# Performance work log

Measured on AMD Instinct MI355X. Metric: run time of the kernel, lower is better.

Reference implementation:

```python
import jax, jax.numpy as jnp
import numpy as np

EPS = 1e-6
R = 2          # filter half-width (length=2 -> 5x5 directional filters)
TAU = 0.1
PI = float(np.pi)

# ---- kernels (all single-channel, OIHW) ----
_SOBEL_X = jnp.array([[-1., 0., 1.], [-2., 0., 2.], [-1., 0., 1.]], dtype=jnp.float32)[None, None] / 8.0  # kornia normalized sobel
_SOBEL_Y = jnp.transpose(_SOBEL_X, (0, 1, 3, 2))

def _gauss_kernel5():
    x = jnp.arange(5, dtype=jnp.float32) - 2.0
    g = jnp.exp(-(x * x) / (2.0 * 4.0))  # sigma = 2
    g = g / g.sum()
    return (g[:, None] * g[None, :])[None, None]  # (1,1,5,5)

def _dir_filters():
    k = 2 * R + 1
    horiz = np.zeros((k, k), np.float32); horiz[R, :] = 1.0
    vert = np.zeros((k, k), np.float32); vert[:, R] = 1.0
    cnt_diag = np.eye(k, dtype=np.float32)
    lead_diag = np.fliplr(np.eye(k)).astype(np.float32)
    return [jnp.asarray(f)[None, None] for f in (horiz, vert, lead_diag, cnt_diag)]

def _conv(x, k, padding):
    # cross-correlation, NCHW / OIHW (matches F.conv2d)
    return jax.lax.conv_general_dilated(x, k, (1, 1), padding,
                                        dimension_numbers=('NCHW', 'OIHW', 'NCHW'))

def _conv_padded(x, k, pad, mode):
    x = jnp.pad(x, ((0, 0), (0, 0), (pad, pad), (pad, pad)), mode=mode)
    return _conv(x, k, 'VALID')

def _normal_angles(img):
    # img: (B,1,H,W). kornia gaussian_blur2d: reflect pad; spatial_gradient: replicate pad.
    blur = _conv_padded(img, _gauss_kernel5(), 2, 'reflect')
    gx = _conv_padded(blur, _SOBEL_X, 1, 'edge')
    gy = _conv_padded(blur, _SOBEL_Y, 1, 'edge')
    grad_xx = _conv_padded(gx, _SOBEL_X, 1, 'edge')
    grad_xy = _conv_padded(gy, _SOBEL_X, 1, 'edge')
    grad_yy = _conv_padded(gy, _SOBEL_Y, 1, 'edge')
    angle = jnp.arctan(grad_yy * jnp.sign(-(grad_xy + EPS)) / (grad_xx + EPS))
    return angle[:, 0]  # (B,H,W)

def _section_masks(a):
    horiz = ((a >= -PI / 8) & (a < PI / 8)).astype(jnp.float32)
    vert = (((a >= 3 * PI / 8) & (a < PI / 2)) | ((a >= -PI / 2) & (a < -3 * PI / 8))).astype(jnp.float32)
    lead = ((a >= PI / 8) & (a < 3 * PI / 8)).astype(jnp.float32)
    cnt = ((a >= -3 * PI / 8) & (a < -PI / 8)).astype(jnp.float32)
    return [horiz, vert, lead, cnt]

def setup_inputs() -> dict:
    key = jax.random.key(0)
    k1, k2 = jax.random.split(key)
    predictions = jax.random.uniform(k1, (1, 1, 2048, 2048), dtype=jnp.float32)
    labels = jax.random.uniform(k2, (1, 2048, 2048), dtype=jnp.float32)
    return {"predictions": predictions, "labels": labels}

def reference(predictions, labels):
    true_angles = _normal_angles(labels[:, None])           # (B,H,W)
    # NOTE: original also computes pred_angles = get_normal_anlges(predictions),
    # but it is dead code (never used), so it is omitted.
    exp_preds = jnp.exp(predictions / TAU)                   # (B,1,H,W)
    masks = _section_masks(true_angles)
    pad = [(R, R), (R, R)]
    loss = jnp.zeros_like(exp_preds)
    for filt, mask in zip(_dir_filters(), masks):
        resp = _conv(exp_preds, filt, pad)                   # zero-padded directional sum
        norm = exp_preds / (resp + EPS)
        loss = loss + jnp.log(norm) * mask                   # mask (B,H,W) broadcasts over channel
    return -jnp.mean(loss)
```

## Files before the change

### kernel.cpp

```cpp
#include <hip/hip_runtime.h>
#include <math.h>

#define HH 2048
#define WW 2048
#define T 8

#define GW0 0.15246914402033867f
#define GW1 0.22184129554377693f
#define GW2 0.25137912086578894f

typedef float f4 __attribute__((ext_vector_type(4)));

struct R8 { float v[8]; };
struct R6 { float v[6]; };

__device__ __forceinline__ R8 hrow(const float* __restrict__ lab, int vr, int xb,
                                   bool edgew, bool le, bool re) {
    int r = vr < 0 ? -vr : (vr >= HH ? 2 * HH - 2 - vr : vr);
    const float* row = lab + (size_t)r * WW;
    f4 A = *(const f4*)(row + max(xb - 4, 0));
    f4 B = *(const f4*)(row + xb);
    f4 C = *(const f4*)(row + min(xb + 4, WW - 4));
    float w[12] = {A.x, A.y, A.z, A.w, B.x, B.y, B.z, B.w, C.x, C.y, C.z, C.w};
    if (edgew) {
        if (le) { w[0] = C.x; w[1] = B.w; w[2] = B.z; w[3] = B.y; }
        if (re) { w[8] = B.z; w[9] = B.y; w[10] = B.x; w[11] = A.w; }
    }
    R8 h;
    #pragma unroll
    for (int j = 0; j < 8; ++j)
        h.v[j] = GW0 * (w[j] + w[j + 4]) + GW1 * (w[j + 1] + w[j + 3]) + GW2 * w[j + 2];
    return h;
}

__device__ __forceinline__ R8 vg(const R8& a, const R8& b, const R8& c, const R8& d, const R8& e_,
                                 bool edgew, bool le, bool re) {
    R8 o;
    #pragma unroll
    for (int j = 0; j < 8; ++j)
        o.v[j] = GW0 * (a.v[j] + e_.v[j]) + GW1 * (b.v[j] + d.v[j]) + GW2 * c.v[j];
    if (edgew) {
        if (le) { o.v[0] = o.v[2]; o.v[1] = o.v[2]; }
        if (re) { o.v[6] = o.v[5]; o.v[7] = o.v[5]; }
    }
    return o;
}

__device__ __forceinline__ void sobel(const R8& u, const R8& m, const R8& d, R6& ox, R6& oy,
                                      bool edgew, bool le, bool re) {
    #pragma unroll
    for (int j = 0; j < 6; ++j) {
        ox.v[j] = ((u.v[j+2] - u.v[j]) + 2.f*(m.v[j+2] - m.v[j]) + (d.v[j+2] - d.v[j])) * 0.125f;
        oy.v[j] = ((d.v[j] - u.v[j]) + 2.f*(d.v[j+1] - u.v[j+1]) + (d.v[j+2] - u.v[j+2])) * 0.125f;
    }
    if (edgew) {
        if (le) { ox.v[0] = ox.v[1]; oy.v[0] = oy.v[1]; }
        if (re) { ox.v[5] = ox.v[4]; oy.v[5] = oy.v[4]; }
    }
}

__device__ __forceinline__ R8 erow(const float* __restrict__ pred, int ry, int xb,
                                   bool edgew, bool le, bool re) {
    R8 o;
    if (ry < 0 || ry >= HH) {
        #pragma unroll
        for (int j = 0; j < 8; ++j) o.v[j] = 0.f;
        return o;
    }
    const float* row = pred + (size_t)ry * WW;
    f4 A = *(const f4*)(row + max(xb - 4, 0));
    f4 B = *(const f4*)(row + xb);
    f4 C = *(const f4*)(row + min(xb + 4, WW - 4));
    float w[8] = {A.z, A.w, B.x, B.y, B.z, B.w, C.x, C.y};
    #pragma unroll
    for (int j = 0; j < 8; ++j) o.v[j] = __expf(w[j] * 10.f);
    if (edgew) {
        if (le) { o.v[0] = 0.f; o.v[1] = 0.f; }
        if (re) { o.v[6] = 0.f; o.v[7] = 0.f; }
    }
    return o;
}

__global__ __launch_bounds__(256, 2) void steal_main(const float* __restrict__ pred,
                                                     const float* __restrict__ lab,
                                                     float* __restrict__ acc) {
    const int lane = threadIdx.x & 63;
    const int wid  = (blockIdx.x << 2) + (threadIdx.x >> 6);
    const int sx = wid & 7;
    const int y0 = (wid >> 3) * T;
    const int xb = sx * 256 + lane * 4;
    const bool edgew = (sx == 0) || (sx == 7);
    const bool le = (sx == 0) && (lane == 0);
    const bool re = (sx == 7) && (lane == 63);

    const float T1f = 0.41421356237309503f;
    const float T3f = 2.41421356237309510f;

    R8 A0 = hrow(lab, y0-4, xb, edgew, le, re);
    R8 A1 = hrow(lab, y0-3, xb, edgew, le, re);
    R8 A2 = hrow(lab, y0-2, xb, edgew, le, re);
    R8 A3 = hrow(lab, y0-1, xb, edgew, le, re);
    R8 H0 = hrow(lab, y0+0, xb, edgew, le, re);
    R8 H1 = hrow(lab, y0+1, xb, edgew, le, re);
    R8 H2 = hrow(lab, y0+2, xb, edgew, le, re);
    R8 H3 = hrow(lab, y0+3, xb, edgew, le, re);
    R8 bm2 = vg(A0, A1, A2, A3, H0, edgew, le, re);
    R8 bm1 = vg(A1, A2, A3, H0, H1, edgew, le, re);
    R8 b0  = vg(A2, A3, H0, H1, H2, edgew, le, re);
    R8 b1  = vg(A3, H0, H1, H2, H3, edgew, le, re);
    R6 gx0, gy0, gx1, gy1;
    if (y0 > 0) {
        sobel(bm2, bm1, b0, gx0, gy0, edgew, le, re);
        sobel(bm1, b0,  b1, gx1, gy1, edgew, le, re);
    } else {
        sobel(b0, b0, b1, gx1, gy1, edgew, le, re);
        gx0 = gx1; gy0 = gy1;
    }
    R8 e0 = erow(pred, y0-2, xb, edgew, le, re);
    R8 e1 = erow(pred, y0-1, xb, edgew, le, re);
    R8 e2 = erow(pred, y0+0, xb, edgew, le, re);
    R8 e3 = erow(pred, y0+1, xb, edgew, le, re);

    float lsum = 0.f;

    for (int i = 0; i < T; ++i) {
        const int y = y0 + i;

        R8 bn;
        if (y + 2 < HH) {
            R8 hn = hrow(lab, y + 4, xb, edgew, le, re);
            bn = vg(H0, H1, H2, H3, hn, edgew, le, re);
            H0 = H1; H1 = H2; H2 = H3; H3 = hn;
        } else bn = b1;

        R6 gxn, gyn;
        if (y + 1 < HH) sobel(b0, b1, bn, gxn, gyn, edgew, le, re);
        else { gxn = gx1; gyn = gy1; }

        R8 en = erow(pred, y + 2, xb, edgew, le, re);

        f4 pc4 = *(const f4*)(pred + (size_t)y * WW + xb);
        float pcv[4] = {pc4.x, pc4.y, pc4.z, pc4.w};

        #pragma unroll
        for (int k = 0; k < 4; ++k) {
            float gxx = ((gx0.v[k+2]-gx0.v[k]) + 2.f*(gx1.v[k+2]-gx1.v[k]) +
                         (gxn.v[k+2]-gxn.v[k])) * 0.125f;
            float gxy = ((gy0.v[k+2]-gy0.v[k]) + 2.f*(gy1.v[k+2]-gy1.v[k]) +
                         (gyn.v[k+2]-gyn.v[k])) * 0.125f;
            float gyy = ((gyn.v[k]-gy0.v[k]) + 2.f*(gyn.v[k+1]-gy0.v[k+1]) +
                         (gyn.v[k+2]-gy0.v[k+2])) * 0.125f;
            float sg = -(gxy + 1e-6f);
            float sgn = (sg > 0.f) ? 1.f : ((sg < 0.f) ? -1.f : 0.f);
            float rt = gyy * sgn * __builtin_amdgcn_rcpf(gxx + 1e-6f);

            float hs  = e2.v[k] + e2.v[k+1] + e2.v[k+2] + e2.v[k+3] + e2.v[k+4];
            float vs  = e0.v[k+2] + e1.v[k+2] + e2.v[k+2] + e3.v[k+2] + en.v[k+2];
            float dls = e0.v[k]   + e1.v[k+1] + e2.v[k+2] + e3.v[k+3] + en.v[k+4];
            float dcs = e0.v[k+4] + e1.v[k+3] + e2.v[k+2] + e3.v[k+1] + en.v[k];

            bool isH = (rt >= -T1f) && (rt < T1f);
            bool isL = (rt >=  T1f) && (rt < T3f);
            bool isC = (rt >= -T3f) && (rt < -T1f);
            bool has = isH || isL || isC || (rt >= T3f) || (rt < -T3f);
            float resp = isH ? hs : (isL ? dls : (isC ? dcs : vs));
            float lv = pcv[k] * 10.f - __logf(resp + 1e-6f);
            lsum += has ? lv : 0.f;
        }

        b0 = b1; b1 = bn;
        gx0 = gx1; gx1 = gxn; gy0 = gy1; gy1 = gyn;
        e0 = e1; e1 = e2; e2 = e3; e3 = en;
    }

    #pragma unroll
    for (int off = 32; off; off >>= 1) lsum += __shfl_down(lsum, off, 64);
    if (lane == 0) acc[wid] = lsum;
}

__global__ __launch_bounds__(256) void steal_finalize(const float* __restrict__ acc,
                                                      float* __restrict__ out, int n) {
    __shared__ double sd[256];
    double a = 0.0;
    int n4 = n >> 2;
    for (int i = threadIdx.x; i < n4; i += 256) {
        f4 v = *(const f4*)(acc + i * 4);
        a += (double)v.x + (double)v.y + (double)v.z + (double)v.w;
    }
    for (int i = (n4 << 2) + threadIdx.x; i < n; i += 256) a += (double)acc[i];
    sd[threadIdx.x] = a;
    __syncthreads();
    for (int s = 128; s > 0; s >>= 1) {
        if (threadIdx.x < s) sd[threadIdx.x] += sd[threadIdx.x + s];
        __syncthreads();
    }
    if (threadIdx.x == 0) out[0] = (float)(-sd[0] / 4194304.0);
}

extern "C" void kernel_launch(void* const* d_in, const int* in_sizes, int n_in,
                              void* d_out, int out_size, void* d_ws, size_t ws_size,
                              hipStream_t stream) {
    const float* pred = (const float*)d_in[0];
    const float* lab  = (const float*)d_in[1];
    float* out = (float*)d_out;
    float* ws  = (float*)d_ws;

    const int nwaves = 8 * (HH / T);
    const int nblocks = nwaves / 4;

    steal_main<<<nblocks, 256, 0, stream>>>(pred, lab, ws);
    steal_finalize<<<1, 256, 0, stream>>>(ws, out, nwaves);
}
```

Before: 36.29 us.

## Stage exp(pred) rows in a per-wave LDS ring buffer and prefetch next rows

Each exp(pred/tau) value is now computed once per row and stored in a per-wave shared-memory ring of 8 rows, with halo entries written by the edge lanes. Previously each lane computed 8 exponentials per row for 4 output pixels. Loads of the next label and prediction rows are issued one iteration ahead, and the loop is fully unrolled. Rows per wave drop from 8 to 4 and the occupancy hint rises to 4 blocks, which roughly doubles the per-wave recomputation of the label blur halo. The centre term now comes from a log of the stored exponential instead of the raw prediction, which adds one log per pixel.

```diff
diff --git a/kernel.cpp b/kernel.cpp
--- a/kernel.cpp
+++ b/kernel.cpp
@@ -3,28 +3,40 @@
 
 #define HH 2048
 #define WW 2048
-#define T 8
+#define T 4
+#define RING_STRIDE 264
+#define RING_F (8 * RING_STRIDE)
 
 #define GW0 0.15246914402033867f
 #define GW1 0.22184129554377693f
 #define GW2 0.25137912086578894f
 
-typedef float f4 __attribute__((ext_vector_type(4)));
+typedef float f2v __attribute__((ext_vector_type(2)));
+typedef float f4  __attribute__((ext_vector_type(4)));
 
 struct R8 { float v[8]; };
 struct R6 { float v[6]; };
-
-__device__ __forceinline__ R8 hrow(const float* __restrict__ lab, int vr, int xb,
-                                   bool edgew, bool le, bool re) {
-    int r = vr < 0 ? -vr : (vr >= HH ? 2 * HH - 2 - vr : vr);
-    const float* row = lab + (size_t)r * WW;
-    f4 A = *(const f4*)(row + max(xb - 4, 0));
-    f4 B = *(const f4*)(row + xb);
-    f4 C = *(const f4*)(row + min(xb + 4, WW - 4));
-    float w[12] = {A.x, A.y, A.z, A.w, B.x, B.y, B.z, B.w, C.x, C.y, C.z, C.w};
+struct Raw { f4 a, b, c; };
+
+__device__ __forceinline__ int reflect_row(int vr) {
+    return vr < 0 ? -vr : (vr >= HH ? 2 * HH - 2 - vr : vr);
+}
+
+__device__ __forceinline__ Raw load_row3(const float* __restrict__ p, int r, int xb) {
+    const float* row = p + (size_t)r * WW;
+    Raw o;
+    o.a = *(const f4*)(row + max(xb - 4, 0));
+    o.b = *(const f4*)(row + xb);
+    o.c = *(const f4*)(row + min(xb + 4, WW - 4));
+    return o;
+}
+
+__device__ __forceinline__ R8 make_h(const Raw& R, bool edgew, bool le, bool re) {
+    float w[12] = {R.a.x, R.a.y, R.a.z, R.a.w, R.b.x, R.b.y, R.b.z, R.b.w,
+                   R.c.x, R.c.y, R.c.z, R.c.w};
     if (edgew) {
-        if (le) { w[0] = C.x; w[1] = B.w; w[2] = B.z; w[3] = B.y; }
-        if (re) { w[8] = B.z; w[9] = B.y; w[10] = B.x; w[11] = A.w; }
+        if (le) { w[0] = R.c.x; w[1] = R.b.w; w[2] = R.b.z; w[3] = R.b.y; }
+        if (re) { w[8] = R.b.z; w[9] = R.b.y; w[10] = R.b.x; w[11] = R.a.w; }
     }
     R8 h;
     #pragma unroll
@@ -59,88 +71,149 @@
     }
 }
 
-__device__ __forceinline__ R8 erow(const float* __restrict__ pred, int ry, int xb,
-                                   bool edgew, bool le, bool re) {
+__device__ __forceinline__ void ewrite(float* __restrict__ ring, int slot, int lane,
+                                       const f4& pv, const f2v& pl, const f2v& pr,
+                                       bool zrow, bool lzero, bool rzero) {
+    float* rp = ring + slot * RING_STRIDE;
+    if (!zrow) {
+        f4 ev;
+        ev.x = __expf(pv.x * 10.f); ev.y = __expf(pv.y * 10.f);
+        ev.z = __expf(pv.z * 10.f); ev.w = __expf(pv.w * 10.f);
+        *(f4*)(rp + 4 + 4 * lane) = ev;
+        if (lane == 0) {
+            f2v h2; h2.x = lzero ? 0.f : __expf(pl.x * 10.f);
+                    h2.y = lzero ? 0.f : __expf(pl.y * 10.f);
+            *(f2v*)(rp + 2) = h2;
+        }
+        if (lane == 63) {
+            f2v h2; h2.x = rzero ? 0.f : __expf(pr.x * 10.f);
+                    h2.y = rzero ? 0.f : __expf(pr.y * 10.f);
+            *(f2v*)(rp + 260) = h2;
+        }
+    } else {
+        f4 z = {0.f, 0.f, 0.f, 0.f};
+        *(f4*)(rp + 4 + 4 * lane) = z;
+        if (lane == 0)  { f2v z2 = {0.f, 0.f}; *(f2v*)(rp + 2) = z2; }
+        if (lane == 63) { f2v z2 = {0.f, 0.f}; *(f2v*)(rp + 260) = z2; }
+    }
+}
+
+__device__ __forceinline__ R8 eread(const float* __restrict__ ring, int slot, int lane) {
+    const float* rp = ring + slot * RING_STRIDE + 4 * lane;
+    f2v w01 = *(const f2v*)(rp + 2);
+    f4  w25 = *(const f4*)(rp + 4);
+    f2v w67 = *(const f2v*)(rp + 8);
     R8 o;
-    if (ry < 0 || ry >= HH) {
-        #pragma unroll
-        for (int j = 0; j < 8; ++j) o.v[j] = 0.f;
-        return o;
-    }
-    const float* row = pred + (size_t)ry * WW;
-    f4 A = *(const f4*)(row + max(xb - 4, 0));
-    f4 B = *(const f4*)(row + xb);
-    f4 C = *(const f4*)(row + min(xb + 4, WW - 4));
-    float w[8] = {A.z, A.w, B.x, B.y, B.z, B.w, C.x, C.y};
-    #pragma unroll
-    for (int j = 0; j < 8; ++j) o.v[j] = __expf(w[j] * 10.f);
-    if (edgew) {
-        if (le) { o.v[0] = 0.f; o.v[1] = 0.f; }
-        if (re) { o.v[6] = 0.f; o.v[7] = 0.f; }
-    }
+    o.v[0] = w01.x; o.v[1] = w01.y; o.v[2] = w25.x; o.v[3] = w25.y;
+    o.v[4] = w25.z; o.v[5] = w25.w; o.v[6] = w67.x; o.v[7] = w67.y;
     return o;
 }
 
-__global__ __launch_bounds__(256, 2) void steal_main(const float* __restrict__ pred,
+__global__ __launch_bounds__(256, 4) void steal_main(const float* __restrict__ pred,
                                                      const float* __restrict__ lab,
                                                      float* __restrict__ acc) {
+    __shared__ float ring_s[4 * RING_F];
     const int lane = threadIdx.x & 63;
-    const int wid  = (blockIdx.x << 2) + (threadIdx.x >> 6);
+    const int warp = threadIdx.x >> 6;
+    const int wid  = (blockIdx.x << 2) + warp;
     const int sx = wid & 7;
     const int y0 = (wid >> 3) * T;
     const int xb = sx * 256 + lane * 4;
     const bool edgew = (sx == 0) || (sx == 7);
     const bool le = (sx == 0) && (lane == 0);
     const bool re = (sx == 7) && (lane == 63);
+    const bool lzero = (sx == 0), rzero = (sx == 7);
+    float* ring = ring_s + warp * RING_F;
 
     const float T1f = 0.41421356237309503f;
     const float T3f = 2.41421356237309510f;
 
-    R8 A0 = hrow(lab, y0-4, xb, edgew, le, re);
-    R8 A1 = hrow(lab, y0-3, xb, edgew, le, re);
-    R8 A2 = hrow(lab, y0-2, xb, edgew, le, re);
-    R8 A3 = hrow(lab, y0-1, xb, edgew, le, re);
-    R8 H0 = hrow(lab, y0+0, xb, edgew, le, re);
-    R8 H1 = hrow(lab, y0+1, xb, edgew, le, re);
-    R8 H2 = hrow(lab, y0+2, xb, edgew, le, re);
-    R8 H3 = hrow(lab, y0+3, xb, edgew, le, re);
-    R8 bm2 = vg(A0, A1, A2, A3, H0, edgew, le, re);
-    R8 bm1 = vg(A1, A2, A3, H0, H1, edgew, le, re);
-    R8 b0  = vg(A2, A3, H0, H1, H2, edgew, le, re);
-    R8 b1  = vg(A3, H0, H1, H2, H3, edgew, le, re);
+    R8 H0, H1, H2, H3, b0, b1;
     R6 gx0, gy0, gx1, gy1;
-    if (y0 > 0) {
-        sobel(bm2, bm1, b0, gx0, gy0, edgew, le, re);
-        sobel(bm1, b0,  b1, gx1, gy1, edgew, le, re);
-    } else {
-        sobel(b0, b0, b1, gx1, gy1, edgew, le, re);
-        gx0 = gx1; gy0 = gy1;
-    }
-    R8 e0 = erow(pred, y0-2, xb, edgew, le, re);
-    R8 e1 = erow(pred, y0-1, xb, edgew, le, re);
-    R8 e2 = erow(pred, y0+0, xb, edgew, le, re);
-    R8 e3 = erow(pred, y0+1, xb, edgew, le, re);
+    {
+        Raw r0 = load_row3(lab, reflect_row(y0 - 4), xb);
+        Raw r1 = load_row3(lab, reflect_row(y0 - 3), xb);
+        Raw r2 = load_row3(lab, reflect_row(y0 - 2), xb);
+        Raw r3 = load_row3(lab, reflect_row(y0 - 1), xb);
+        R8 A0 = make_h(r0, edgew, le, re);
+        R8 A1 = make_h(r1, edgew, le, re);
+        R8 A2 = make_h(r2, edgew, le, re);
+        R8 A3 = make_h(r3, edgew, le, re);
+        Raw r4 = load_row3(lab, y0 + 0, xb);
+        Raw r5 = load_row3(lab, y0 + 1, xb);
+        Raw r6 = load_row3(lab, y0 + 2, xb);
+        Raw r7 = load_row3(lab, y0 + 3, xb);
+        H0 = make_h(r4, edgew, le, re);
+        H1 = make_h(r5, edgew, le, re);
+        H2 = make_h(r6, edgew, le, re);
+        H3 = make_h(r7, edgew, le, re);
+        R8 bm2 = vg(A0, A1, A2, A3, H0, edgew, le, re);
+        R8 bm1 = vg(A1, A2, A3, H0, H1, edgew, le, re);
+        b0 = vg(A2, A3, H0, H1, H2, edgew, le, re);
+        b1 = vg(A3, H0, H1, H2, H3, edgew, le, re);
+        if (y0 > 0) {
+            sobel(bm2, bm1, b0, gx0, gy0, edgew, le, re);
+            sobel(bm1, b0,  b1, gx1, gy1, edgew, le, re);
+        } else {
+            sobel(b0, b0, b1, gx1, gy1, edgew, le, re);
+            gx0 = gx1; gy0 = gy1;
+        }
+    }
+
+    #pragma unroll
+    for (int j = 0; j < 4; ++j) {
+        int ry = y0 - 2 + j;
+        bool zrow = (ry < 0);
+        const float* prow = pred + (size_t)max(ry, 0) * WW;
+        f4 pv = *(const f4*)(prow + xb);
+        f2v pl = {0.f, 0.f}, pr = {0.f, 0.f};
+        if (lane == 0)  pl = *(const f2v*)(prow + max(xb - 2, 0));
+        if (lane == 63) pr = *(const f2v*)(prow + min(xb + 4, WW - 2));
+        ewrite(ring, (ry + 4) & 7, lane, pv, pl, pr, zrow, lzero, rzero);
+    }
+
+    Raw nlab = load_row3(lab, reflect_row(y0 + 4), xb);
+    f4 npred; f2v npl = {0.f, 0.f}, npr = {0.f, 0.f};
+    {
+        const float* prow = pred + (size_t)min(y0 + 2, HH - 1) * WW;
+        npred = *(const f4*)(prow + xb);
+        if (lane == 0)  npl = *(const f2v*)(prow + max(xb - 2, 0));
+        if (lane == 63) npr = *(const f2v*)(prow + min(xb + 4, WW - 2));
+    }
 
     float lsum = 0.f;
 
+    #pragma unroll
     for (int i = 0; i < T; ++i) {
         const int y = y0 + i;
 
         R8 bn;
         if (y + 2 < HH) {
-            R8 hn = hrow(lab, y + 4, xb, edgew, le, re);
+            R8 hn = make_h(nlab, edgew, le, re);
             bn = vg(H0, H1, H2, H3, hn, edgew, le, re);
             H0 = H1; H1 = H2; H2 = H3; H3 = hn;
         } else bn = b1;
 
+        ewrite(ring, (y + 6) & 7, lane, npred, npl, npr, (y + 2 >= HH), lzero, rzero);
+
+        if (i < T - 1) {
+            nlab = load_row3(lab, reflect_row(y + 5), xb);
+            const float* prow = pred + (size_t)min(y + 3, HH - 1) * WW;
+            npred = *(const f4*)(prow + xb);
+            npl.x = 0.f; npl.y = 0.f; npr.x = 0.f; npr.y = 0.f;
+            if (lane == 0)  npl = *(const f2v*)(prow + max(xb - 2, 0));
+            if (lane == 63) npr = *(const f2v*)(prow + min(xb + 4, WW - 2));
+        }
+
         R6 gxn, gyn;
         if (y + 1 < HH) sobel(b0, b1, bn, gxn, gyn, edgew, le, re);
         else { gxn = gx1; gyn = gy1; }
 
-        R8 en = erow(pred, y + 2, xb, edgew, le, re);
-
-        f4 pc4 = *(const f4*)(pred + (size_t)y * WW + xb);
-        float pcv[4] = {pc4.x, pc4.y, pc4.z, pc4.w};
+        R8 wA = eread(ring, (y + 2) & 7, lane);
+        R8 wB = eread(ring, (y + 3) & 7, lane);
+        R8 wC = eread(ring, (y + 4) & 7, lane);
+        R8 wD = eread(ring, (y + 5) & 7, lane);
+        R8 wE = eread(ring, (y + 6) & 7, lane);
 
         #pragma unroll
         for (int k = 0; k < 4; ++k) {
@@ -154,23 +227,23 @@
             float sgn = (sg > 0.f) ? 1.f : ((sg < 0.f) ? -1.f : 0.f);
             float rt = gyy * sgn * __builtin_amdgcn_rcpf(gxx + 1e-6f);
 
-            float hs  = e2.v[k] + e2.v[k+1] + e2.v[k+2] + e2.v[k+3] + e2.v[k+4];
-            float vs  = e0.v[k+2] + e1.v[k+2] + e2.v[k+2] + e3.v[k+2] + en.v[k+2];
-            float dls = e0.v[k]   + e1.v[k+1] + e2.v[k+2] + e3.v[k+3] + en.v[k+4];
-            float dcs = e0.v[k+4] + e1.v[k+3] + e2.v[k+2] + e3.v[k+1] + en.v[k];
+            float hs  = wC.v[k] + wC.v[k+1] + wC.v[k+2] + wC.v[k+3] + wC.v[k+4];
+            float vs  = wA.v[k+2] + wB.v[k+2] + wC.v[k+2] + wD.v[k+2] + wE.v[k+2];
+            float dls = wA.v[k]   + wB.v[k+1] + wC.v[k+2] + wD.v[k+3] + wE.v[k+4];
+            float dcs = wA.v[k+4] + wB.v[k+3] + wC.v[k+2] + wD.v[k+1] + wE.v[k];
 
             bool isH = (rt >= -T1f) && (rt < T1f);
             bool isL = (rt >=  T1f) && (rt < T3f);
             bool isC = (rt >= -T3f) && (rt < -T1f);
             bool has = isH || isL || isC || (rt >= T3f) || (rt < -T3f);
             float resp = isH ? hs : (isL ? dls : (isC ? dcs : vs));
-            float lv = pcv[k] * 10.f - __logf(resp + 1e-6f);
+            float lc = __logf(wC.v[k+2]);
+            float lv = lc - __logf(resp + 1e-6f);
             lsum += has ? lv : 0.f;
         }
 
         b0 = b1; b1 = bn;
         gx0 = gx1; gx1 = gxn; gy0 = gy1; gy1 = gyn;
-        e0 = e1; e1 = e2; e2 = e3; e3 = en;
     }
 
     #pragma unroll
```

Measured after the change: 133.5 us. +268.0%, slower.

## Split fused kernel into section-code pass and loss pass with smaller row tiles

Applied to the files above, without the earlier changes.

Breaks the single fused kernel into two. The first computes the blur, Hessian and angle section per pixel and writes a byte code to workspace. The second reads those codes together with the predictions to compute the directional sums and the log loss. The row tile also drops from 8 to 4, which doubles the number of waves and the halo recomputation. The intent is lower register pressure and more parallelism per kernel, at the cost of an extra 4 MB write and read of the codes and one more kernel launch.

```diff
diff --git a/kernel.cpp b/kernel.cpp
--- a/kernel.cpp
+++ b/kernel.cpp
@@ -1,30 +1,41 @@
 #include <hip/hip_runtime.h>
 #include <math.h>
+#include <stdint.h>
 
 #define HH 2048
 #define WW 2048
-#define T 8
+#define T 4
 
 #define GW0 0.15246914402033867f
 #define GW1 0.22184129554377693f
 #define GW2 0.25137912086578894f
 
-typedef float f4 __attribute__((ext_vector_type(4)));
+typedef float f2v __attribute__((ext_vector_type(2)));
+typedef float f4  __attribute__((ext_vector_type(4)));
 
 struct R8 { float v[8]; };
 struct R6 { float v[6]; };
-
-__device__ __forceinline__ R8 hrow(const float* __restrict__ lab, int vr, int xb,
-                                   bool edgew, bool le, bool re) {
-    int r = vr < 0 ? -vr : (vr >= HH ? 2 * HH - 2 - vr : vr);
-    const float* row = lab + (size_t)r * WW;
-    f4 A = *(const f4*)(row + max(xb - 4, 0));
-    f4 B = *(const f4*)(row + xb);
-    f4 C = *(const f4*)(row + min(xb + 4, WW - 4));
-    float w[12] = {A.x, A.y, A.z, A.w, B.x, B.y, B.z, B.w, C.x, C.y, C.z, C.w};
-    if (edgew) {
-        if (le) { w[0] = C.x; w[1] = B.w; w[2] = B.z; w[3] = B.y; }
-        if (re) { w[8] = B.z; w[9] = B.y; w[10] = B.x; w[11] = A.w; }
+struct Raw { f4 a, b, c; };
+
+__device__ __forceinline__ int reflect_row(int vr) {
+    return vr < 0 ? -vr : (vr >= HH ? 2 * HH - 2 - vr : vr);
+}
+
+__device__ __forceinline__ Raw load_row3(const float* __restrict__ p, int r, int xb) {
+    const float* row = p + (size_t)r * WW;
+    Raw o;
+    o.a = *(const f4*)(row + max(xb - 4, 0));
+    o.b = *(const f4*)(row + xb);
+    o.c = *(const f4*)(row + min(xb + 4, WW - 4));
+    return o;
+}
+
+__device__ __forceinline__ R8 make_h(const Raw& R, bool edgew, bool le, bool re) {
+    float w[12] = {R.a.x, R.a.y, R.a.z, R.a.w, R.b.x, R.b.y, R.b.z, R.b.w,
+                   R.c.x, R.c.y, R.c.z, R.c.w};
+    if (edgew) {
+        if (le) { w[0] = R.c.x; w[1] = R.b.w; w[2] = R.b.z; w[3] = R.b.y; }
+        if (re) { w[8] = R.b.z; w[9] = R.b.y; w[10] = R.b.x; w[11] = R.a.w; }
     }
     R8 h;
     #pragma unroll
@@ -81,9 +92,8 @@
     return o;
 }
 
-__global__ __launch_bounds__(256, 2) void steal_main(const float* __restrict__ pred,
-                                                     const float* __restrict__ lab,
-                                                     float* __restrict__ acc) {
+__global__ __launch_bounds__(256) void steal_sections(const float* __restrict__ lab,
+                                                      uint32_t* __restrict__ codes) {
     const int lane = threadIdx.x & 63;
     const int wid  = (blockIdx.x << 2) + (threadIdx.x >> 6);
     const int sx = wid & 7;
@@ -96,39 +106,45 @@
     const float T1f = 0.41421356237309503f;
     const float T3f = 2.41421356237309510f;
 
-    R8 A0 = hrow(lab, y0-4, xb, edgew, le, re);
-    R8 A1 = hrow(lab, y0-3, xb, edgew, le, re);
-    R8 A2 = hrow(lab, y0-2, xb, edgew, le, re);
-    R8 A3 = hrow(lab, y0-1, xb, edgew, le, re);
-    R8 H0 = hrow(lab, y0+0, xb, edgew, le, re);
-    R8 H1 = hrow(lab, y0+1, xb, edgew, le, re);
-    R8 H2 = hrow(lab, y0+2, xb, edgew, le, re);
-    R8 H3 = hrow(lab, y0+3, xb, edgew, le, re);
-    R8 bm2 = vg(A0, A1, A2, A3, H0, edgew, le, re);
-    R8 bm1 = vg(A1, A2, A3, H0, H1, edgew, le, re);
-    R8 b0  = vg(A2, A3, H0, H1, H2, edgew, le, re);
-    R8 b1  = vg(A3, H0, H1, H2, H3, edgew, le, re);
+    R8 H0, H1, H2, H3, b0, b1;
     R6 gx0, gy0, gx1, gy1;
-    if (y0 > 0) {
-        sobel(bm2, bm1, b0, gx0, gy0, edgew, le, re);
-        sobel(bm1, b0,  b1, gx1, gy1, edgew, le, re);
-    } else {
-        sobel(b0, b0, b1, gx1, gy1, edgew, le, re);
-        gx0 = gx1; gy0 = gy1;
-    }
-    R8 e0 = erow(pred, y0-2, xb, edgew, le, re);
-    R8 e1 = erow(pred, y0-1, xb, edgew, le, re);
-    R8 e2 = erow(pred, y0+0, xb, edgew, le, re);
-    R8 e3 = erow(pred, y0+1, xb, edgew, le, re);
-
-    float lsum = 0.f;
-
+    {
+        Raw r0 = load_row3(lab, reflect_row(y0 - 4), xb);
+        Raw r1 = load_row3(lab, reflect_row(y0 - 3), xb);
+        Raw r2 = load_row3(lab, reflect_row(y0 - 2), xb);
+        Raw r3 = load_row3(lab, reflect_row(y0 - 1), xb);
+        R8 A0 = make_h(r0, edgew, le, re);
+        R8 A1 = make_h(r1, edgew, le, re);
+        R8 A2 = make_h(r2, edgew, le, re);
+        R8 A3 = make_h(r3, edgew, le, re);
+        Raw r4 = load_row3(lab, y0 + 0, xb);
+        Raw r5 = load_row3(lab, y0 + 1, xb);
+        Raw r6 = load_row3(lab, y0 + 2, xb);
+        Raw r7 = load_row3(lab, y0 + 3, xb);
+        H0 = make_h(r4, edgew, le, re);
+        H1 = make_h(r5, edgew, le, re);
+        H2 = make_h(r6, edgew, le, re);
+        H3 = make_h(r7, edgew, le, re);
+        R8 bm2 = vg(A0, A1, A2, A3, H0, edgew, le, re);
+        R8 bm1 = vg(A1, A2, A3, H0, H1, edgew, le, re);
+        b0 = vg(A2, A3, H0, H1, H2, edgew, le, re);
+        b1 = vg(A3, H0, H1, H2, H3, edgew, le, re);
+        if (y0 > 0) {
+            sobel(bm2, bm1, b0, gx0, gy0, edgew, le, re);
+            sobel(bm1, b0,  b1, gx1, gy1, edgew, le, re);
+        } else {
+            sobel(b0, b0, b1, gx1, gy1, edgew, le, re);
+            gx0 = gx1; gy0 = gy1;
+        }
+    }
+
+    #pragma unroll
     for (int i = 0; i < T; ++i) {
         const int y = y0 + i;
 
         R8 bn;
         if (y + 2 < HH) {
-            R8 hn = hrow(lab, y + 4, xb, edgew, le, re);
+            R8 hn = make_h(load_row3(lab, reflect_row(y + 4), xb), edgew, le, re);
             bn = vg(H0, H1, H2, H3, hn, edgew, le, re);
             H0 = H1; H1 = H2; H2 = H3; H3 = hn;
         } else bn = b1;
@@ -137,11 +153,7 @@
         if (y + 1 < HH) sobel(b0, b1, bn, gxn, gyn, edgew, le, re);
         else { gxn = gx1; gyn = gy1; }
 
-        R8 en = erow(pred, y + 2, xb, edgew, le, re);
-
-        f4 pc4 = *(const f4*)(pred + (size_t)y * WW + xb);
-        float pcv[4] = {pc4.x, pc4.y, pc4.z, pc4.w};
-
+        uint32_t cw = 0;
         #pragma unroll
         for (int k = 0; k < 4; ++k) {
             float gxx = ((gx0.v[k+2]-gx0.v[k]) + 2.f*(gx1.v[k+2]-gx1.v[k]) +
@@ -154,22 +166,61 @@
             float sgn = (sg > 0.f) ? 1.f : ((sg < 0.f) ? -1.f : 0.f);
             float rt = gyy * sgn * __builtin_amdgcn_rcpf(gxx + 1e-6f);
 
+            bool isH = (rt >= -T1f) && (rt < T1f);
+            bool isL = (rt >=  T1f) && (rt < T3f);
+            bool isC = (rt >= -T3f) && (rt < -T1f);
+            bool isV = (rt >= T3f) || (rt < -T3f);
+            uint32_t c = isH ? 0u : (isL ? 1u : (isC ? 2u : (isV ? 3u : 4u)));
+            cw |= c << (8 * k);
+        }
+        codes[((size_t)y * WW + xb) >> 2] = cw;
+
+        b0 = b1; b1 = bn;
+        gx0 = gx1; gx1 = gxn; gy0 = gy1; gy1 = gyn;
+    }
+}
+
+__global__ __launch_bounds__(256) void steal_loss(const float* __restrict__ pred,
+                                                  const uint32_t* __restrict__ codes,
+                                                  float* __restrict__ acc) {
+    const int lane = threadIdx.x & 63;
+    const int wid  = (blockIdx.x << 2) + (threadIdx.x >> 6);
+    const int sx = wid & 7;
+    const int y0 = (wid >> 3) * T;
+    const int xb = sx * 256 + lane * 4;
+    const bool edgew = (sx == 0) || (sx == 7);
+    const bool le = (sx == 0) && (lane == 0);
+    const bool re = (sx == 7) && (lane == 63);
+
+    R8 e0 = erow(pred, y0 - 2, xb, edgew, le, re);
+    R8 e1 = erow(pred, y0 - 1, xb, edgew, le, re);
+    R8 e2 = erow(pred, y0 + 0, xb, edgew, le, re);
+    R8 e3 = erow(pred, y0 + 1, xb, edgew, le, re);
+
+    float lsum = 0.f;
+
+    #pragma unroll
+    for (int i = 0; i < T; ++i) {
+        const int y = y0 + i;
+        R8 en = erow(pred, y + 2, xb, edgew, le, re);
+
+        f4 pc4 = *(const f4*)(pred + (size_t)y * WW + xb);
+        float pcv[4] = {pc4.x, pc4.y, pc4.z, pc4.w};
+        uint32_t cw = codes[((size_t)y * WW + xb) >> 2];
+
+        #pragma unroll
+        for (int k = 0; k < 4; ++k) {
             float hs  = e2.v[k] + e2.v[k+1] + e2.v[k+2] + e2.v[k+3] + e2.v[k+4];
             float vs  = e0.v[k+2] + e1.v[k+2] + e2.v[k+2] + e3.v[k+2] + en.v[k+2];
             float dls = e0.v[k]   + e1.v[k+1] + e2.v[k+2] + e3.v[k+3] + en.v[k+4];
             float dcs = e0.v[k+4] + e1.v[k+3] + e2.v[k+2] + e3.v[k+1] + en.v[k];
 
-            bool isH = (rt >= -T1f) && (rt < T1f);
-            bool isL = (rt >=  T1f) && (rt < T3f);
-            bool isC = (rt >= -T3f) && (rt < -T1f);
-            bool has = isH || isL || isC || (rt >= T3f) || (rt < -T3f);
-            float resp = isH ? hs : (isL ? dls : (isC ? dcs : vs));
+            uint32_t c = (cw >> (8 * k)) & 0xffu;
+            float resp = (c == 0u) ? hs : ((c == 1u) ? dls : ((c == 2u) ? dcs : vs));
             float lv = pcv[k] * 10.f - __logf(resp + 1e-6f);
-            lsum += has ? lv : 0.f;
+            lsum += (c < 4u) ? lv : 0.f;
         }
 
-        b0 = b1; b1 = bn;
-        gx0 = gx1; gx1 = gxn; gy0 = gy1; gy1 = gyn;
         e0 = e1; e1 = e2; e2 = e3; e3 = en;
     }
 
@@ -203,11 +254,14 @@
     const float* pred = (const float*)d_in[0];
     const float* lab  = (const float*)d_in[1];
     float* out = (float*)d_out;
-    float* ws  = (float*)d_ws;
+
+    uint32_t* codes = (uint32_t*)d_ws;
+    float* accb = (float*)((uint8_t*)d_ws + (size_t)HH * WW);
 
     const int nwaves = 8 * (HH / T);
     const int nblocks = nwaves / 4;
 
-    steal_main<<<nblocks, 256, 0, stream>>>(pred, lab, ws);
-    steal_finalize<<<1, 256, 0, stream>>>(ws, out, nwaves);
-}
+    steal_sections<<<nblocks, 256, 0, stream>>>(lab, codes);
+    steal_loss<<<nblocks, 256, 0, stream>>>(pred, codes, accb);
+    steal_finalize<<<1, 256, 0, stream>>>(accb, out, nwaves);
+}
```

New measurement: 41.33 us. +13.9%, slower.

## Split into interior kernel without boundary checks and separate border kernel

Applied to the files above, without the earlier changes.

Moves the 4 top and 4 bottom rows into a small border kernel, so the interior kernel runs a fully unrolled 16-step software pipeline with no reflect or bounds branches and rotating register buffers. Sobel and the 3x3 second derivatives are factored into separable partial sums, and the horizontal 5-tap sum uses prefix sums to cut adds. This adds a third kernel launch and may raise register pressure because the launch_bounds occupancy hint was dropped.

```diff
diff --git a/kernel.cpp b/kernel.cpp
--- a/kernel.cpp
+++ b/kernel.cpp
@@ -3,7 +3,6 @@
 
 #define HH 2048
 #define WW 2048
-#define T 8
 
 #define GW0 0.15246914402033867f
 #define GW1 0.22184129554377693f
@@ -11,20 +10,20 @@
 
 typedef float f4 __attribute__((ext_vector_type(4)));
 
+#define NWI 2040
+#define NWB 16
+#define NACC (NWI + NWB)
+
 struct R8 { float v[8]; };
 struct R6 { float v[6]; };
-
-__device__ __forceinline__ R8 hrow(const float* __restrict__ lab, int vr, int xb,
-                                   bool edgew, bool le, bool re) {
-    int r = vr < 0 ? -vr : (vr >= HH ? 2 * HH - 2 - vr : vr);
-    const float* row = lab + (size_t)r * WW;
-    f4 A = *(const f4*)(row + max(xb - 4, 0));
-    f4 B = *(const f4*)(row + xb);
-    f4 C = *(const f4*)(row + min(xb + 4, WW - 4));
-    float w[12] = {A.x, A.y, A.z, A.w, B.x, B.y, B.z, B.w, C.x, C.y, C.z, C.w};
-    if (edgew) {
-        if (le) { w[0] = C.x; w[1] = B.w; w[2] = B.z; w[3] = B.y; }
-        if (re) { w[8] = B.z; w[9] = B.y; w[10] = B.x; w[11] = A.w; }
+struct Raw { f4 a, b, c; };
+
+__device__ __forceinline__ R8 make_h(const Raw& R, bool edgew, bool le, bool re) {
+    float w[12] = {R.a.x, R.a.y, R.a.z, R.a.w, R.b.x, R.b.y, R.b.z, R.b.w,
+                   R.c.x, R.c.y, R.c.z, R.c.w};
+    if (edgew) {
+        if (le) { w[0] = R.c.x; w[1] = R.b.w; w[2] = R.b.z; w[3] = R.b.y; }
+        if (re) { w[8] = R.b.z; w[9] = R.b.y; w[10] = R.b.x; w[11] = R.a.w; }
     }
     R8 h;
     #pragma unroll
@@ -33,8 +32,8 @@
     return h;
 }
 
-__device__ __forceinline__ R8 vg(const R8& a, const R8& b, const R8& c, const R8& d, const R8& e_,
-                                 bool edgew, bool le, bool re) {
+__device__ __forceinline__ R8 vg5(const R8& a, const R8& b, const R8& c, const R8& d, const R8& e_,
+                                  bool edgew, bool le, bool re) {
     R8 o;
     #pragma unroll
     for (int j = 0; j < 8; ++j)
@@ -46,8 +45,157 @@
     return o;
 }
 
-__device__ __forceinline__ void sobel(const R8& u, const R8& m, const R8& d, R6& ox, R6& oy,
-                                      bool edgew, bool le, bool re) {
+__device__ __forceinline__ void sobel1(const R8& u, const R8& m, const R8& d, R6& ox, R6& oy,
+                                       bool edgew, bool le, bool re) {
+    float E[8], F[8];
+    #pragma unroll
+    for (int j = 0; j < 8; ++j) {
+        E[j] = u.v[j] + 2.f * m.v[j] + d.v[j];
+        F[j] = d.v[j] - u.v[j];
+    }
+    #pragma unroll
+    for (int j = 0; j < 6; ++j) {
+        ox.v[j] = (E[j + 2] - E[j]) * 0.125f;
+        oy.v[j] = (F[j] + 2.f * F[j + 1] + F[j + 2]) * 0.125f;
+    }
+    if (edgew) {
+        if (le) { ox.v[0] = ox.v[1]; oy.v[0] = oy.v[1]; }
+        if (re) { ox.v[5] = ox.v[4]; oy.v[5] = oy.v[4]; }
+    }
+}
+
+__global__ __launch_bounds__(256) void steal_interior(const float* __restrict__ pred,
+                                                      const float* __restrict__ lab,
+                                                      float* __restrict__ acc) {
+    const int lane = threadIdx.x & 63;
+    const int wid  = (blockIdx.x << 2) + (threadIdx.x >> 6);
+    const int w  = wid & 7;
+    const int rg = wid >> 3;
+    const int y0 = 4 + rg * 8;
+    const int xb = w * 256 + lane * 4;
+    const int xl = max(xb - 4, 0);
+    const int xr = min(xb + 4, WW - 4);
+    const bool edgew = (w == 0) || (w == 7);
+    const bool le = (w == 0) && (lane == 0);
+    const bool re = (w == 7) && (lane == 63);
+
+    const float T1f = 0.41421356237309503f;
+    const float T3f = 2.41421356237309510f;
+
+    R8 h[5], bl[3], er[5];
+    R6 gzx[3], gzy[3];
+    float lsum = 0.f;
+
+    #pragma unroll
+    for (int s = 0; s < 16; ++s) {
+        {
+            const float* row = lab + (size_t)(y0 - 4 + s) * WW;
+            Raw rw;
+            rw.a = *(const f4*)(row + xl);
+            rw.b = *(const f4*)(row + xb);
+            rw.c = *(const f4*)(row + xr);
+            h[s % 5] = make_h(rw, edgew, le, re);
+        }
+
+        if (s >= 4) {
+            const int j = s - 4;
+            bl[j % 3] = vg5(h[j % 5], h[(j + 1) % 5], h[(j + 2) % 5],
+                            h[(j + 3) % 5], h[(j + 4) % 5], edgew, le, re);
+            const float* row = pred + (size_t)(y0 - 2 + j) * WW;
+            f4 A = *(const f4*)(row + xl);
+            f4 B = *(const f4*)(row + xb);
+            f4 C = *(const f4*)(row + xr);
+            float ww[8] = {A.z, A.w, B.x, B.y, B.z, B.w, C.x, C.y};
+            R8 e_;
+            #pragma unroll
+            for (int q = 0; q < 8; ++q) e_.v[q] = __expf(ww[q] * 10.f);
+            if (edgew) {
+                if (le) { e_.v[0] = 0.f; e_.v[1] = 0.f; }
+                if (re) { e_.v[6] = 0.f; e_.v[7] = 0.f; }
+            }
+            er[j % 5] = e_;
+        }
+
+        if (s >= 6) {
+            const int g = s - 6;
+            sobel1(bl[g % 3], bl[(g + 1) % 3], bl[(g + 2) % 3],
+                   gzx[g % 3], gzy[g % 3], edgew, le, re);
+        }
+
+        if (s >= 8) {
+            const int i = s - 8;
+            const R6& X0 = gzx[i % 3];
+            const R6& X1 = gzx[(i + 1) % 3];
+            const R6& X2 = gzx[(i + 2) % 3];
+            const R6& Y0 = gzy[i % 3];
+            const R6& Y1 = gzy[(i + 1) % 3];
+            const R6& Y2 = gzy[(i + 2) % 3];
+            float Cx[6], Cy[6], Dy[6];
+            #pragma unroll
+            for (int j = 0; j < 6; ++j) {
+                Cx[j] = X0.v[j] + 2.f * X1.v[j] + X2.v[j];
+                Cy[j] = Y0.v[j] + 2.f * Y1.v[j] + Y2.v[j];
+                Dy[j] = Y2.v[j] - Y0.v[j];
+            }
+            const R8& eA = er[i % 5];
+            const R8& eB = er[(i + 1) % 5];
+            const R8& eC = er[(i + 2) % 5];
+            const R8& eD = er[(i + 3) % 5];
+            const R8& eE = er[(i + 4) % 5];
+            float P[8];
+            P[0] = eC.v[0];
+            #pragma unroll
+            for (int j = 1; j < 8; ++j) P[j] = P[j - 1] + eC.v[j];
+
+            f4 pc4 = *(const f4*)(pred + (size_t)(y0 + i) * WW + xb);
+            float pcv[4] = {pc4.x, pc4.y, pc4.z, pc4.w};
+
+            #pragma unroll
+            for (int k = 0; k < 4; ++k) {
+                float gxx = (Cx[k + 2] - Cx[k]) * 0.125f;
+                float gxy = (Cy[k + 2] - Cy[k]) * 0.125f;
+                float gyy = (Dy[k] + 2.f * Dy[k + 1] + Dy[k + 2]) * 0.125f;
+
+                float sg = -(gxy + 1e-6f);
+                float sgn = (sg > 0.f) ? 1.f : ((sg < 0.f) ? -1.f : 0.f);
+                float rt = gyy * sgn * __builtin_amdgcn_rcpf(gxx + 1e-6f);
+
+                float hs  = (k == 0) ? P[4] : (P[k + 4] - P[k - 1]);
+                float vs  = eA.v[k+2] + eB.v[k+2] + eC.v[k+2] + eD.v[k+2] + eE.v[k+2];
+                float dls = eA.v[k]   + eB.v[k+1] + eC.v[k+2] + eD.v[k+3] + eE.v[k+4];
+                float dcs = eA.v[k+4] + eB.v[k+3] + eC.v[k+2] + eD.v[k+1] + eE.v[k];
+
+                bool isH = (rt >= -T1f) && (rt < T1f);
+                bool isL = (rt >=  T1f) && (rt < T3f);
+                bool isC = (rt >= -T3f) && (rt < -T1f);
+                bool has = isH || isL || isC || (rt >= T3f) || (rt < -T3f);
+                float resp = isH ? hs : (isL ? dls : (isC ? dcs : vs));
+                float lv = pcv[k] * 10.f - __logf(resp + 1e-6f);
+                lsum += has ? lv : 0.f;
+            }
+        }
+    }
+
+    #pragma unroll
+    for (int off = 32; off; off >>= 1) lsum += __shfl_down(lsum, off, 64);
+    if (lane == 0) acc[wid] = lsum;
+}
+
+__device__ __forceinline__ int reflect_row(int vr) {
+    return vr < 0 ? -vr : (vr >= HH ? 2 * HH - 2 - vr : vr);
+}
+
+__device__ __forceinline__ Raw load_row3(const float* __restrict__ p, int r, int xb) {
+    const float* row = p + (size_t)r * WW;
+    Raw o;
+    o.a = *(const f4*)(row + max(xb - 4, 0));
+    o.b = *(const f4*)(row + xb);
+    o.c = *(const f4*)(row + min(xb + 4, WW - 4));
+    return o;
+}
+
+__device__ __forceinline__ void sobelB(const R8& u, const R8& m, const R8& d, R6& ox, R6& oy,
+                                       bool edgew, bool le, bool re) {
     #pragma unroll
     for (int j = 0; j < 6; ++j) {
         ox.v[j] = ((u.v[j+2] - u.v[j]) + 2.f*(m.v[j+2] - m.v[j]) + (d.v[j+2] - d.v[j])) * 0.125f;
@@ -59,8 +207,8 @@
     }
 }
 
-__device__ __forceinline__ R8 erow(const float* __restrict__ pred, int ry, int xb,
-                                   bool edgew, bool le, bool re) {
+__device__ __forceinline__ R8 erowB(const float* __restrict__ pred, int ry, int xb,
+                                    bool edgew, bool le, bool re) {
     R8 o;
     if (ry < 0 || ry >= HH) {
         #pragma unroll
@@ -81,13 +229,13 @@
     return o;
 }
 
-__global__ __launch_bounds__(256, 2) void steal_main(const float* __restrict__ pred,
-                                                     const float* __restrict__ lab,
-                                                     float* __restrict__ acc) {
+__global__ __launch_bounds__(256) void steal_border(const float* __restrict__ pred,
+                                                    const float* __restrict__ lab,
+                                                    float* __restrict__ acc) {
     const int lane = threadIdx.x & 63;
-    const int wid  = (blockIdx.x << 2) + (threadIdx.x >> 6);
-    const int sx = wid & 7;
-    const int y0 = (wid >> 3) * T;
+    const int b = (blockIdx.x << 2) + (threadIdx.x >> 6);
+    const int sx = b & 7;
+    const int y0 = (b >> 3) ? 2044 : 0;
     const int xb = sx * 256 + lane * 4;
     const bool edgew = (sx == 0) || (sx == 7);
     const bool le = (sx == 0) && (lane == 0);
@@ -96,48 +244,53 @@
     const float T1f = 0.41421356237309503f;
     const float T3f = 2.41421356237309510f;
 
-    R8 A0 = hrow(lab, y0-4, xb, edgew, le, re);
-    R8 A1 = hrow(lab, y0-3, xb, edgew, le, re);
-    R8 A2 = hrow(lab, y0-2, xb, edgew, le, re);
-    R8 A3 = hrow(lab, y0-1, xb, edgew, le, re);
-    R8 H0 = hrow(lab, y0+0, xb, edgew, le, re);
-    R8 H1 = hrow(lab, y0+1, xb, edgew, le, re);
-    R8 H2 = hrow(lab, y0+2, xb, edgew, le, re);
-    R8 H3 = hrow(lab, y0+3, xb, edgew, le, re);
-    R8 bm2 = vg(A0, A1, A2, A3, H0, edgew, le, re);
-    R8 bm1 = vg(A1, A2, A3, H0, H1, edgew, le, re);
-    R8 b0  = vg(A2, A3, H0, H1, H2, edgew, le, re);
-    R8 b1  = vg(A3, H0, H1, H2, H3, edgew, le, re);
+    R8 H0, H1, H2, H3, b0, b1;
     R6 gx0, gy0, gx1, gy1;
-    if (y0 > 0) {
-        sobel(bm2, bm1, b0, gx0, gy0, edgew, le, re);
-        sobel(bm1, b0,  b1, gx1, gy1, edgew, le, re);
-    } else {
-        sobel(b0, b0, b1, gx1, gy1, edgew, le, re);
-        gx0 = gx1; gy0 = gy1;
-    }
-    R8 e0 = erow(pred, y0-2, xb, edgew, le, re);
-    R8 e1 = erow(pred, y0-1, xb, edgew, le, re);
-    R8 e2 = erow(pred, y0+0, xb, edgew, le, re);
-    R8 e3 = erow(pred, y0+1, xb, edgew, le, re);
+    {
+        R8 A0 = make_h(load_row3(lab, reflect_row(y0 - 4), xb), edgew, le, re);
+        R8 A1 = make_h(load_row3(lab, reflect_row(y0 - 3), xb), edgew, le, re);
+        R8 A2 = make_h(load_row3(lab, reflect_row(y0 - 2), xb), edgew, le, re);
+        R8 A3 = make_h(load_row3(lab, reflect_row(y0 - 1), xb), edgew, le, re);
+        H0 = make_h(load_row3(lab, y0 + 0, xb), edgew, le, re);
+        H1 = make_h(load_row3(lab, y0 + 1, xb), edgew, le, re);
+        H2 = make_h(load_row3(lab, y0 + 2, xb), edgew, le, re);
+        H3 = make_h(load_row3(lab, y0 + 3, xb), edgew, le, re);
+        R8 bm2 = vg5(A0, A1, A2, A3, H0, edgew, le, re);
+        R8 bm1 = vg5(A1, A2, A3, H0, H1, edgew, le, re);
+        b0 = vg5(A2, A3, H0, H1, H2, edgew, le, re);
+        b1 = vg5(A3, H0, H1, H2, H3, edgew, le, re);
+        if (y0 > 0) {
+            sobelB(bm2, bm1, b0, gx0, gy0, edgew, le, re);
+            sobelB(bm1, b0,  b1, gx1, gy1, edgew, le, re);
+        } else {
+            sobelB(b0, b0, b1, gx1, gy1, edgew, le, re);
+            gx0 = gx1; gy0 = gy1;
+        }
+    }
+
+    R8 e0 = erowB(pred, y0 - 2, xb, edgew, le, re);
+    R8 e1 = erowB(pred, y0 - 1, xb, edgew, le, re);
+    R8 e2 = erowB(pred, y0 + 0, xb, edgew, le, re);
+    R8 e3 = erowB(pred, y0 + 1, xb, edgew, le, re);
 
     float lsum = 0.f;
 
-    for (int i = 0; i < T; ++i) {
+    #pragma unroll
+    for (int i = 0; i < 4; ++i) {
         const int y = y0 + i;
 
         R8 bn;
         if (y + 2 < HH) {
-            R8 hn = hrow(lab, y + 4, xb, edgew, le, re);
-            bn = vg(H0, H1, H2, H3, hn, edgew, le, re);
+            R8 hn = make_h(load_row3(lab, reflect_row(y + 4), xb), edgew, le, re);
+            bn = vg5(H0, H1, H2, H3, hn, edgew, le, re);
             H0 = H1; H1 = H2; H2 = H3; H3 = hn;
         } else bn = b1;
 
         R6 gxn, gyn;
-        if (y + 1 < HH) sobel(b0, b1, bn, gxn, gyn, edgew, le, re);
+        if (y + 1 < HH) sobelB(b0, b1, bn, gxn, gyn, edgew, le, re);
         else { gxn = gx1; gyn = gy1; }
 
-        R8 en = erow(pred, y + 2, xb, edgew, le, re);
+        R8 en = erowB(pred, y + 2, xb, edgew, le, re);
 
         f4 pc4 = *(const f4*)(pred + (size_t)y * WW + xb);
         float pcv[4] = {pc4.x, pc4.y, pc4.z, pc4.w};
@@ -175,7 +328,7 @@
 
     #pragma unroll
     for (int off = 32; off; off >>= 1) lsum += __shfl_down(lsum, off, 64);
-    if (lane == 0) acc[wid] = lsum;
+    if (lane == 0) acc[NWI + b] = lsum;
 }
 
 __global__ __launch_bounds__(256) void steal_finalize(const float* __restrict__ acc,
@@ -205,9 +358,7 @@
     float* out = (float*)d_out;
     float* ws  = (float*)d_ws;
 
-    const int nwaves = 8 * (HH / T);
-    const int nblocks = nwaves / 4;
-
-    steal_main<<<nblocks, 256, 0, stream>>>(pred, lab, ws);
-    steal_finalize<<<1, 256, 0, stream>>>(ws, out, nwaves);
-}
+    steal_border<<<NWB / 4, 256, 0, stream>>>(pred, lab, ws);
+    steal_interior<<<NWI / 4, 256, 0, stream>>>(pred, lab, ws);
+    steal_finalize<<<1, 256, 0, stream>>>(ws, out, NACC);
+}
```

After: 61.55 us. +69.6%, slower.
